# Performance work log

Hardware: AMD Instinct MI355X
Metric: run time of the kernel (lower is better)

The kernel has to match this reference:

```python
import jax, jax.numpy as jnp
import numpy as np

NUM_CLASSES = 21
THRESH = 0.5
VAR = (0.1, 0.2)
B, P, O = 128, 8732, 16

def setup_inputs() -> dict:
    key = jax.random.key(0)
    ks = jax.random.split(key, 7)
    loc_preds = jax.random.normal(ks[0], (B, P, 4), jnp.float32)
    score_preds = jax.random.normal(ks[1], (B, P, NUM_CLASSES), jnp.float32)
    # priors in center-size form (cx, cy, w, h)
    pc = jax.random.uniform(ks[2], (P, 2), minval=0.05, maxval=0.95)
    pwh = jax.random.uniform(ks[3], (P, 2), minval=0.05, maxval=0.4)
    priors = jnp.concatenate([pc, pwh], axis=1).astype(jnp.float32)
    # ground truth: valid point-form boxes + label in last column
    gc = jax.random.uniform(ks[4], (B, O, 2), minval=0.2, maxval=0.8)
    gwh = jax.random.uniform(ks[5], (B, O, 2), minval=0.05, maxval=0.3)
    boxes = jnp.concatenate([gc - gwh / 2, gc + gwh / 2], axis=-1)
    labels = jax.random.randint(ks[6], (B, O, 1), 1, NUM_CLASSES).astype(jnp.float32)
    gt_data = jnp.concatenate([boxes, labels], axis=-1).astype(jnp.float32)
    return {"loc_preds": loc_preds, "score_preds": score_preds,
            "gt_data": gt_data, "priors": priors}

def _iou(a, b):
    # a: (O,4) point form, b: (P,4) point form -> (O,P)
    lt = jnp.maximum(a[:, None, :2], b[None, :, :2])
    rb = jnp.minimum(a[:, None, 2:], b[None, :, 2:])
    wh = jnp.clip(rb - lt, 0.0)
    inter = wh[..., 0] * wh[..., 1]
    area_a = (a[:, 2] - a[:, 0]) * (a[:, 3] - a[:, 1])
    area_b = (b[:, 2] - b[:, 0]) * (b[:, 3] - b[:, 1])
    return inter / (area_a[:, None] + area_b[None, :] - inter)

def _encode(matched, priors):
    # matched: (P,4) point form; priors: (P,4) center-size form
    g_c = (matched[:, :2] + matched[:, 2:]) / 2 - priors[:, :2]
    g_c = g_c / (VAR[0] * priors[:, 2:])
    g_wh = (matched[:, 2:] - matched[:, :2]) / priors[:, 2:]
    g_wh = jnp.log(g_wh) / VAR[1]
    return jnp.concatenate([g_c, g_wh], axis=1)

def _match_one(gt_loc, gt_cls, priors_pt, priors):
    ious = _iou(gt_loc, priors_pt)                    # (O, P)
    best_prior_idx = jnp.argmax(ious, axis=1)         # (O,)
    best_truth_overlap = jnp.max(ious, axis=0)        # (P,)
    best_truth_idx = jnp.argmax(ious, axis=0)         # (P,)
    # ensure every gt's best prior is kept positive and assigned to that gt
    best_truth_overlap = best_truth_overlap.at[best_prior_idx].set(2.0)
    best_truth_idx = best_truth_idx.at[best_prior_idx].set(jnp.arange(gt_loc.shape[0]))
    matched = gt_loc[best_truth_idx]                  # (P, 4)
    conf = gt_cls[best_truth_idx]
    conf = jnp.where(best_truth_overlap < THRESH, 0.0, conf)
    return _encode(matched, priors), conf.astype(jnp.int32)

def reference(loc_preds, score_preds, gt_data, priors):
    priors_pt = jnp.concatenate([priors[:, :2] - priors[:, 2:] / 2,
                                 priors[:, :2] + priors[:, 2:] / 2], axis=1)
    gt_loc, gt_cls = gt_data[..., :4], gt_data[..., 4]
    loc_targets, score_targets = jax.vmap(
        lambda l, c: _match_one(l, c, priors_pt, priors))(gt_loc, gt_cls)
    pos = score_targets > 0                           # (B, P)
    num_matched = jnp.sum(pos).astype(jnp.float32)

    # SmoothL1 over positive boxes (sum reduction)
    d = jnp.abs(loc_preds - loc_targets)
    sl1 = jnp.where(d < 1.0, 0.5 * d * d, d - 0.5)    # (B, P, 4)
    loc_loss = jnp.sum(jnp.where(pos[..., None], sl1, 0.0))

    # per-box cross-entropy on all boxes
    lse = jax.nn.logsumexp(score_preds, axis=-1)      # (B, P)
    gathered = jnp.take_along_axis(score_preds, score_targets[..., None],
                                   axis=-1)[..., 0]
    ce = lse - gathered                               # (B, P)

    # hard negative mining via double argsort ranking
    mine = jnp.where(pos, 0.0, ce)
    idx = jnp.argsort(-mine, axis=1)
    rank = jnp.argsort(idx, axis=1)
    num_pos = jnp.sum(pos, axis=1)                    # (B,)
    total_pos = jnp.sum(num_pos)
    num_neg = jnp.minimum(3 * num_pos, P - total_pos - 1)
    neg = rank < num_neg[:, None]

    sel = pos | neg
    conf_loss = jnp.sum(jnp.where(sel, ce, 0.0))
    return loc_loss / num_matched, conf_loss / num_matched
```

## Files before the change

### kernel.cpp

```cpp
#include <hip/hip_runtime.h>
#include <cstdint>
#include <cstddef>

#define B 128
#define P 8732
#define NC 21
#define O 16
#define THRESH 0.5f
#define QPI 2183
#define NBX 9
#define NPART (B * NBX)
#define NB1 8

typedef unsigned long long u64;
typedef unsigned int u32;
typedef unsigned char u8;

__device__ __forceinline__ float iou_pt(float a0, float a1, float a2, float a3,
                                        float b0, float b1, float b2, float b3) {
    float ltx = fmaxf(a0, b0), lty = fmaxf(a1, b1);
    float rbx = fminf(a2, b2), rby = fminf(a3, b3);
    float wx = fmaxf(rbx - ltx, 0.0f), wy = fmaxf(rby - lty, 0.0f);
    float inter = wx * wy;
    float aa = (a2 - a0) * (a3 - a1);
    float ab = (b2 - b0) * (b3 - b1);
    return inter / (aa + ab - inter);
}

__global__ void __launch_bounds__(256) k_pass1(const float* __restrict__ gt,
                                               const float* __restrict__ priors,
                                               u64* __restrict__ bk,
                                               u8* __restrict__ bidx) {
    const int b = blockIdx.y;
    __shared__ float s_gt[O * 4];
    __shared__ u64 s_wk[4][O];
    const int tid = threadIdx.x;
    const int wave = tid >> 6, lane = tid & 63;
    if (tid < O * 4) {
        int o = tid >> 2, c = tid & 3;
        s_gt[tid] = gt[(b * O + o) * 5 + c];
    }
    __syncthreads();

    u64 lk[O];
#pragma unroll
    for (int o = 0; o < O; o++) lk[o] = 0ull;

    for (int p = blockIdx.x * 256 + tid; p < P; p += NB1 * 256) {
        float4 pr = reinterpret_cast<const float4*>(priors)[p];
        float b0 = pr.x - pr.z * 0.5f, b1 = pr.y - pr.w * 0.5f;
        float b2 = pr.x + pr.z * 0.5f, b3 = pr.y + pr.w * 0.5f;
        float bov = -1.0f; int bo = 0;
#pragma unroll
        for (int o = 0; o < O; o++) {
            float v = iou_pt(s_gt[o * 4 + 0], s_gt[o * 4 + 1], s_gt[o * 4 + 2], s_gt[o * 4 + 3],
                             b0, b1, b2, b3);
            u64 key = ((u64)__float_as_uint(v) << 32) | (u64)(0xFFFFFFFFu - (u32)p);
            lk[o] = (key > lk[o]) ? key : lk[o];
            if (v > bov) { bov = v; bo = o; }
        }
        bidx[(size_t)b * P + p] = (u8)(bo | ((bov >= THRESH) ? 0x80 : 0));
    }

#pragma unroll
    for (int o = 0; o < O; o++) {
        u64 k = lk[o];
#pragma unroll
        for (int off = 32; off > 0; off >>= 1) {
            u64 other = (u64)__shfl_xor((long long)k, off, 64);
            k = (other > k) ? other : k;
        }
        if (lane == 0) s_wk[wave][o] = k;
    }
    __syncthreads();
    if (tid < O) {
        u64 k = s_wk[0][tid];
#pragma unroll
        for (int w = 1; w < 4; w++) { u64 v = s_wk[w][tid]; k = (v > k) ? v : k; }
        bk[((size_t)b * O + tid) * NB1 + blockIdx.x] = k;
    }
}

__global__ void __launch_bounds__(256) k_pass2(const float* __restrict__ gt,
                                               const float* __restrict__ priors,
                                               const u64* __restrict__ bk,
                                               const u8* __restrict__ bidx,
                                               const float* __restrict__ loc_preds,
                                               const float* __restrict__ scores,
                                               float* __restrict__ mine,
                                               double* __restrict__ pl,
                                               double* __restrict__ pc,
                                               int* __restrict__ pn) {
    const int b = blockIdx.y;
    __shared__ float s_gt[O * 5];
    __shared__ int s_bp[O];
    const int tid = threadIdx.x;
    if (tid < O * 5) s_gt[tid] = gt[b * O * 5 + tid];
    if (tid < O) {
        u64 k = bk[((size_t)b * O + tid) * NB1];
#pragma unroll
        for (int i = 1; i < NB1; i++) {
            u64 v = bk[((size_t)b * O + tid) * NB1 + i];
            k = (v > k) ? v : k;
        }
        s_bp[tid] = (int)(0xFFFFFFFFu - (u32)(k & 0xFFFFFFFFull));
    }
    __syncthreads();

    const int gq = blockIdx.x * 256 + tid;
    double l_loc = 0.0, l_ce = 0.0;
    int l_np = 0;

    if (gq < QPI) {
        const int p0 = gq * 4;
        float fs[84];
        const float4* s4 = reinterpret_cast<const float4*>(scores)
                           + (size_t)b * (size_t)(P * NC / 4) + (size_t)21 * gq;
#pragma unroll
        for (int i = 0; i < 21; i++) {
            float4 v = s4[i];
            fs[4 * i + 0] = v.x; fs[4 * i + 1] = v.y;
            fs[4 * i + 2] = v.z; fs[4 * i + 3] = v.w;
        }
        const u32 mw = *reinterpret_cast<const u32*>(bidx + (size_t)b * P + p0);
        float4 pr4[4];
#pragma unroll
        for (int j = 0; j < 4; j++) pr4[j] = reinterpret_cast<const float4*>(priors)[p0 + j];

        float mine_v[4];

#pragma unroll
        for (int j = 0; j < 4; j++) {
            const int p = p0 + j;
            const float4 pr = pr4[j];

            int e = (int)((mw >> (8 * j)) & 0xFFu);
            int best_idx = e & 0x3F;
            bool matched = (e & 0x80) != 0;
#pragma unroll
            for (int o = 0; o < O; o++) {
                if (s_bp[o] == p) { best_idx = o; matched = true; }
            }
            int cls = matched ? (int)s_gt[best_idx * 5 + 4] : 0;

            float mx = fs[21 * j];
#pragma unroll
            for (int c = 1; c < NC; c++) mx = fmaxf(mx, fs[21 * j + c]);
            float se = 0.0f;
#pragma unroll
            for (int c = 0; c < NC; c++) se += __expf(fs[21 * j + c] - mx);
            float lse = mx + __logf(se);
            float g = fs[21 * j];
#pragma unroll
            for (int c = 1; c < NC; c++) g = (c == cls) ? fs[21 * j + c] : g;
            float ce = lse - g;

            bool pos = cls > 0;
            mine_v[j] = pos ? 0.0f : ce;

            if (pos) {
                l_np++;
                l_ce += (double)ce;
                float m0 = s_gt[best_idx * 5 + 0], m1 = s_gt[best_idx * 5 + 1];
                float m2 = s_gt[best_idx * 5 + 2], m3 = s_gt[best_idx * 5 + 3];
                float tx = ((m0 + m2) * 0.5f - pr.x) / (0.1f * pr.z);
                float ty = ((m1 + m3) * 0.5f - pr.y) / (0.1f * pr.w);
                float tw = __logf((m2 - m0) / pr.z) * 5.0f;
                float th = __logf((m3 - m1) / pr.w) * 5.0f;
                float4 lp = reinterpret_cast<const float4*>(loc_preds)[(size_t)b * P + p];
                float d0 = fabsf(lp.x - tx), d1 = fabsf(lp.y - ty);
                float d2 = fabsf(lp.z - tw), d3 = fabsf(lp.w - th);
                float s0 = d0 < 1.0f ? 0.5f * d0 * d0 : d0 - 0.5f;
                float s1 = d1 < 1.0f ? 0.5f * d1 * d1 : d1 - 0.5f;
                float s2 = d2 < 1.0f ? 0.5f * d2 * d2 : d2 - 0.5f;
                float s3 = d3 < 1.0f ? 0.5f * d3 * d3 : d3 - 0.5f;
                l_loc += (double)(s0 + s1 + s2 + s3);
            }
        }
        float4 mv = make_float4(mine_v[0], mine_v[1], mine_v[2], mine_v[3]);
        reinterpret_cast<float4*>(mine)[((size_t)b * P + p0) >> 2] = mv;
    }

    const int lane = tid & 63;
    const int wave = tid >> 6;
#pragma unroll
    for (int off = 32; off > 0; off >>= 1) {
        l_loc += __shfl_xor(l_loc, off, 64);
        l_ce  += __shfl_xor(l_ce, off, 64);
        l_np  += __shfl_xor(l_np, off, 64);
    }
    __shared__ double s_loc[4], s_ce[4];
    __shared__ int s_np[4];
    if (lane == 0) { s_loc[wave] = l_loc; s_ce[wave] = l_ce; s_np[wave] = l_np; }
    __syncthreads();
    if (tid == 0) {
        int q = b * NBX + blockIdx.x;
        pl[q] = (s_loc[0] + s_loc[1]) + (s_loc[2] + s_loc[3]);
        pc[q] = (s_ce[0] + s_ce[1]) + (s_ce[2] + s_ce[3]);
        pn[q] = s_np[0] + s_np[1] + s_np[2] + s_np[3];
    }
}

__global__ void __launch_bounds__(1024) k_hardneg(const float* __restrict__ mine,
                                                  const int* __restrict__ pn,
                                                  double* __restrict__ pneg) {
    const int b = blockIdx.x;
    const int tid = threadIdx.x;
    const int lane = tid & 63, wave = tid >> 6;
    __shared__ float s_mine[P];
    __shared__ u32 s_hist[256];
    __shared__ u32 s_sel[2];
    __shared__ double s_red[16];
    __shared__ int s_ti[16];
    __shared__ int s_np9[NBX];
    __shared__ int s_k;

    {
        int t = 0;
        for (int i = tid; i < NPART; i += 1024) t += pn[i];
#pragma unroll
        for (int off = 32; off > 0; off >>= 1) t += __shfl_xor(t, off, 64);
        if (lane == 0) s_ti[wave] = t;
    }
    if (tid < NBX) s_np9[tid] = pn[b * NBX + tid];
    __syncthreads();
    if (tid == 0) {
        int tp = 0;
#pragma unroll
        for (int w = 0; w < 16; w++) tp += s_ti[w];
        int np = 0;
#pragma unroll
        for (int x = 0; x < NBX; x++) np += s_np9[x];
        int k = 3 * np;
        int cap = P - tp - 1;
        if (cap < k) k = cap;
        s_k = k;
    }
    __syncthreads();
    const int k = s_k;

    if (k <= 0) {
        if (tid == 0) pneg[b] = 0.0;
        return;
    }

    for (int i = tid; i < P; i += 1024) s_mine[i] = mine[(size_t)b * P + i];
    if (tid == 0) { s_sel[0] = 0u; s_sel[1] = (u32)k; }
    __syncthreads();

    for (int shift = 24; shift >= 0; shift -= 8) {
        if (tid < 256) s_hist[tid] = 0u;
        __syncthreads();
        u32 prefix = s_sel[0];
        u32 kr = s_sel[1];
        u32 himask = (shift == 24) ? 0u : (0xFFFFFFFFu << (shift + 8));
        for (int i = tid; i < P; i += 1024) {
            u32 v = __float_as_uint(s_mine[i]);
            if ((v & himask) == prefix) atomicAdd(&s_hist[(v >> shift) & 255u], 1u);
        }
        __syncthreads();
        if (tid < 64) {
            const int L = tid;
            const int btop = 255 - 4 * L;
            u32 h0 = s_hist[btop], h1 = s_hist[btop - 1], h2 = s_hist[btop - 2], h3 = s_hist[btop - 3];
            u32 g4 = h0 + h1 + h2 + h3;
            u32 x = g4;
#pragma unroll
            for (int off = 1; off < 64; off <<= 1) {
                u32 v = __shfl_up(x, off, 64);
                if (L >= off) x += v;
            }
            u32 excl = x - g4;
            if (excl < kr && excl + g4 >= kr) {
                u32 c = excl; int chosen = btop; u32 kloc = kr;
                u32 nc;
                nc = c + h0; if (c < kr && nc >= kr) { chosen = btop;     kloc = kr - c; } c = nc;
                nc = c + h1; if (c < kr && nc >= kr) { chosen = btop - 1; kloc = kr - c; } c = nc;
                nc = c + h2; if (c < kr && nc >= kr) { chosen = btop - 2; kloc = kr - c; } c = nc;
                nc = c + h3; if (c < kr && nc >= kr) { chosen = btop - 3; kloc = kr - c; } c = nc;
                s_sel[0] = prefix | ((u32)chosen << shift);
                s_sel[1] = kloc;
            }
        }
        __syncthreads();
    }

    u32 tbits = s_sel[0];
    u32 kr = s_sel[1];
    float T = __uint_as_float(tbits);

    double sd = 0.0;
    for (int i = tid; i < P; i += 1024) {
        u32 v = __float_as_uint(s_mine[i]);
        if (v > tbits) sd += (double)s_mine[i];
    }
#pragma unroll
    for (int off = 32; off > 0; off >>= 1) sd += __shfl_xor(sd, off, 64);
    if (lane == 0) s_red[wave] = sd;
    __syncthreads();
    if (tid == 0) {
        double tt = 0.0;
#pragma unroll
        for (int w = 0; w < 16; w++) tt += s_red[w];
        pneg[b] = tt + (double)kr * (double)T;
    }
}

__global__ void __launch_bounds__(1024) k_fin(const double* __restrict__ pl,
                                              const double* __restrict__ pc,
                                              const int* __restrict__ pn,
                                              const double* __restrict__ pneg,
                                              float* __restrict__ out) {
    const int tid = threadIdx.x;
    const int lane = tid & 63, wave = tid >> 6;
    __shared__ double s_l[16], s_c[16], s_g[16];
    __shared__ int s_t[16];

    double tl = 0.0, tc = 0.0, tg = 0.0;
    int tn = 0;
    for (int i = tid; i < NPART; i += 1024) { tl += pl[i]; tc += pc[i]; tn += pn[i]; }
    if (tid < B) tg = pneg[tid];
#pragma unroll
    for (int off = 32; off > 0; off >>= 1) {
        tl += __shfl_xor(tl, off, 64);
        tc += __shfl_xor(tc, off, 64);
        tg += __shfl_xor(tg, off, 64);
        tn += __shfl_xor(tn, off, 64);
    }
    if (lane == 0) { s_l[wave] = tl; s_c[wave] = tc; s_g[wave] = tg; s_t[wave] = tn; }
    __syncthreads();
    if (tid == 0) {
        double al = 0.0, ac = 0.0, ag = 0.0;
        int an = 0;
#pragma unroll
        for (int w = 0; w < 16; w++) { al += s_l[w]; ac += s_c[w]; ag += s_g[w]; an += s_t[w]; }
        double n = (double)an;
        out[0] = (float)(al / n);
        out[1] = (float)((ac + ag) / n);
    }
}

extern "C" void kernel_launch(void* const* d_in, const int* in_sizes, int n_in,
                              void* d_out, int out_size, void* d_ws, size_t ws_size,
                              hipStream_t stream) {
    const float* loc_preds = (const float*)d_in[0];
    const float* scores    = (const float*)d_in[1];
    const float* gt        = (const float*)d_in[2];
    const float* priors    = (const float*)d_in[3];

    char* ws = (char*)d_ws;
    u64* bk      = (u64*)ws;
    double* pl   = (double*)(ws + 131072);
    double* pc   = (double*)(ws + 140288);
    int* pn      = (int*)(ws + 149504);
    double* pneg = (double*)(ws + 154112);
    u8* bidx     = (u8*)(ws + 155136);
    float* mine  = (float*)(ws + 1272832);


    k_pass1<<<dim3(NB1, B), dim3(256), 0, stream>>>(gt, priors, bk, bidx);
    k_pass2<<<dim3(NBX, B), dim3(256), 0, stream>>>(
        gt, priors, bk, bidx, loc_preds, scores, mine, pl, pc, pn);
    k_hardneg<<<dim3(B), dim3(1024), 0, stream>>>(mine, pn, pneg);
    k_fin<<<dim3(1), dim3(1024), 0, stream>>>(pl, pc, pn, pneg, (float*)d_out);
}
```

Baseline: 59.41 us.

## Stage score slabs into LDS with double-buffered async global_load_lds in pass2

Reworks k_pass2 so each wave owns a contiguous run of priors and streams the score rows for 64 priors at a time into per-wave LDS double buffers via global_load_lds. The next chunk's load is issued while the current one is computed. Each lane now handles one prior instead of four, which cuts register pressure from the 84-float array. The aim is better coalescing and overlap of the dominant score read. The cost is extra LDS traffic, manual waitcnt handling, and fewer blocks (6 per batch instead of 9).

Result: no change. 58.27 us (-1.9%).

```diff
diff --git a/kernel.cpp b/kernel.cpp
--- a/kernel.cpp
+++ b/kernel.cpp
@@ -7,10 +7,12 @@
 #define NC 21
 #define O 16
 #define THRESH 0.5f
-#define QPI 2183
-#define NBX 9
-#define NPART (B * NBX)
 #define NB1 8
+#define NBX2 6
+#define BPB 1456
+#define WPW 364
+#define NPART (B * NBX2)
+#define SLABF 1536
 
 typedef unsigned long long u64;
 typedef unsigned int u32;
@@ -81,6 +83,21 @@
     }
 }
 
+__device__ __forceinline__ void stage64(const float* __restrict__ gsrc,
+                                        float* lds, int nf4, int lane) {
+    const char* src = (const char*)gsrc;
+    char* dst = (char*)lds;
+#pragma unroll
+    for (int i = 0; i < 6; i++) {
+        int idx = i * 64 + lane;
+        if (idx >= nf4) idx = nf4 - 1;
+        __builtin_amdgcn_global_load_lds(
+            (const __attribute__((address_space(1))) u32*)(src + (size_t)idx * 16),
+            (__attribute__((address_space(3))) u32*)(dst + i * 1024),
+            16, 0, 0);
+    }
+}
+
 __global__ void __launch_bounds__(256) k_pass2(const float* __restrict__ gt,
                                                const float* __restrict__ priors,
                                                const u64* __restrict__ bk,
@@ -92,9 +109,12 @@
                                                double* __restrict__ pc,
                                                int* __restrict__ pn) {
     const int b = blockIdx.y;
+    const int tid = threadIdx.x;
+    const int wave = tid >> 6, lane = tid & 63;
+    __shared__ float s_slab[4][2][SLABF];
     __shared__ float s_gt[O * 5];
     __shared__ int s_bp[O];
-    const int tid = threadIdx.x;
+
     if (tid < O * 5) s_gt[tid] = gt[b * O * 5 + tid];
     if (tid < O) {
         u64 k = bk[((size_t)b * O + tid) * NB1];
@@ -107,82 +127,88 @@
     }
     __syncthreads();
 
-    const int gq = blockIdx.x * 256 + tid;
+    const int wbase = blockIdx.x * BPB + wave * WPW;
+    int wp = P - wbase; if (wp > WPW) wp = WPW;
+    const int nchunk = (wp > 0) ? ((wp + 63) >> 6) : 0;
+
     double l_loc = 0.0, l_ce = 0.0;
     int l_np = 0;
 
-    if (gq < QPI) {
-        const int p0 = gq * 4;
-        float fs[84];
-        const float4* s4 = reinterpret_cast<const float4*>(scores)
-                           + (size_t)b * (size_t)(P * NC / 4) + (size_t)21 * gq;
-#pragma unroll
-        for (int i = 0; i < 21; i++) {
-            float4 v = s4[i];
-            fs[4 * i + 0] = v.x; fs[4 * i + 1] = v.y;
-            fs[4 * i + 2] = v.z; fs[4 * i + 3] = v.w;
-        }
-        const u32 mw = *reinterpret_cast<const u32*>(bidx + (size_t)b * P + p0);
-        float4 pr4[4];
-#pragma unroll
-        for (int j = 0; j < 4; j++) pr4[j] = reinterpret_cast<const float4*>(priors)[p0 + j];
-
-        float mine_v[4];
-
-#pragma unroll
-        for (int j = 0; j < 4; j++) {
-            const int p = p0 + j;
-            const float4 pr = pr4[j];
-
-            int e = (int)((mw >> (8 * j)) & 0xFFu);
-            int best_idx = e & 0x3F;
-            bool matched = (e & 0x80) != 0;
-#pragma unroll
-            for (int o = 0; o < O; o++) {
-                if (s_bp[o] == p) { best_idx = o; matched = true; }
+    if (nchunk > 0) {
+        {
+            int nv0 = wp < 64 ? wp : 64;
+            stage64(scores + ((size_t)b * P + wbase) * NC,
+                    &s_slab[wave][0][0], nv0 * 21 / 4, lane);
+        }
+        for (int c = 0; c < nchunk; ++c) {
+            const int base = wbase + c * 64;
+            int nv = wp - c * 64; if (nv > 64) nv = 64;
+
+            if (c + 1 < nchunk) {
+                int nv2 = wp - (c + 1) * 64; if (nv2 > 64) nv2 = 64;
+                asm volatile("s_waitcnt lgkmcnt(0)" ::: "memory");
+                stage64(scores + ((size_t)b * P + base + 64) * NC,
+                        &s_slab[wave][(c + 1) & 1][0], nv2 * 21 / 4, lane);
+                asm volatile("s_waitcnt vmcnt(6)" ::: "memory");
+            } else {
+                asm volatile("s_waitcnt vmcnt(0)" ::: "memory");
             }
-            int cls = matched ? (int)s_gt[best_idx * 5 + 4] : 0;
-
-            float mx = fs[21 * j];
-#pragma unroll
-            for (int c = 1; c < NC; c++) mx = fmaxf(mx, fs[21 * j + c]);
-            float se = 0.0f;
-#pragma unroll
-            for (int c = 0; c < NC; c++) se += __expf(fs[21 * j + c] - mx);
-            float lse = mx + __logf(se);
-            float g = fs[21 * j];
-#pragma unroll
-            for (int c = 1; c < NC; c++) g = (c == cls) ? fs[21 * j + c] : g;
-            float ce = lse - g;
-
-            bool pos = cls > 0;
-            mine_v[j] = pos ? 0.0f : ce;
-
-            if (pos) {
-                l_np++;
-                l_ce += (double)ce;
-                float m0 = s_gt[best_idx * 5 + 0], m1 = s_gt[best_idx * 5 + 1];
-                float m2 = s_gt[best_idx * 5 + 2], m3 = s_gt[best_idx * 5 + 3];
-                float tx = ((m0 + m2) * 0.5f - pr.x) / (0.1f * pr.z);
-                float ty = ((m1 + m3) * 0.5f - pr.y) / (0.1f * pr.w);
-                float tw = __logf((m2 - m0) / pr.z) * 5.0f;
-                float th = __logf((m3 - m1) / pr.w) * 5.0f;
-                float4 lp = reinterpret_cast<const float4*>(loc_preds)[(size_t)b * P + p];
-                float d0 = fabsf(lp.x - tx), d1 = fabsf(lp.y - ty);
-                float d2 = fabsf(lp.z - tw), d3 = fabsf(lp.w - th);
-                float s0 = d0 < 1.0f ? 0.5f * d0 * d0 : d0 - 0.5f;
-                float s1 = d1 < 1.0f ? 0.5f * d1 * d1 : d1 - 0.5f;
-                float s2 = d2 < 1.0f ? 0.5f * d2 * d2 : d2 - 0.5f;
-                float s3 = d3 < 1.0f ? 0.5f * d3 * d3 : d3 - 0.5f;
-                l_loc += (double)(s0 + s1 + s2 + s3);
+            __builtin_amdgcn_sched_barrier(0);
+
+            if (lane < nv) {
+                const int p = base + lane;
+                const float* fsl = &s_slab[wave][c & 1][lane * NC];
+                float fs[NC];
+#pragma unroll
+                for (int cc = 0; cc < NC; cc++) fs[cc] = fsl[cc];
+
+                int e = (int)bidx[(size_t)b * P + p];
+                int best_idx = e & 0x3F;
+                bool matched = (e & 0x80) != 0;
+#pragma unroll
+                for (int o = 0; o < O; o++) {
+                    if (s_bp[o] == p) { best_idx = o; matched = true; }
+                }
+                int cls = matched ? (int)s_gt[best_idx * 5 + 4] : 0;
+
+                float mx = fs[0];
+#pragma unroll
+                for (int cc = 1; cc < NC; cc++) mx = fmaxf(mx, fs[cc]);
+                float se = 0.0f;
+#pragma unroll
+                for (int cc = 0; cc < NC; cc++) se += __expf(fs[cc] - mx);
+                float lse = mx + __logf(se);
+                float g = fs[0];
+#pragma unroll
+                for (int cc = 1; cc < NC; cc++) g = (cc == cls) ? fs[cc] : g;
+                float ce = lse - g;
+
+                bool pos = cls > 0;
+                mine[(size_t)b * P + p] = pos ? 0.0f : ce;
+
+                if (pos) {
+                    l_np++;
+                    l_ce += (double)ce;
+                    float4 pr = reinterpret_cast<const float4*>(priors)[p];
+                    float m0 = s_gt[best_idx * 5 + 0], m1 = s_gt[best_idx * 5 + 1];
+                    float m2 = s_gt[best_idx * 5 + 2], m3 = s_gt[best_idx * 5 + 3];
+                    float tx = ((m0 + m2) * 0.5f - pr.x) / (0.1f * pr.z);
+                    float ty = ((m1 + m3) * 0.5f - pr.y) / (0.1f * pr.w);
+                    float tw = __logf((m2 - m0) / pr.z) * 5.0f;
+                    float th = __logf((m3 - m1) / pr.w) * 5.0f;
+                    float4 lp = reinterpret_cast<const float4*>(loc_preds)[(size_t)b * P + p];
+                    float d0 = fabsf(lp.x - tx), d1 = fabsf(lp.y - ty);
+                    float d2 = fabsf(lp.z - tw), d3 = fabsf(lp.w - th);
+                    float s0 = d0 < 1.0f ? 0.5f * d0 * d0 : d0 - 0.5f;
+                    float s1 = d1 < 1.0f ? 0.5f * d1 * d1 : d1 - 0.5f;
+                    float s2 = d2 < 1.0f ? 0.5f * d2 * d2 : d2 - 0.5f;
+                    float s3 = d3 < 1.0f ? 0.5f * d3 * d3 : d3 - 0.5f;
+                    l_loc += (double)((s0 + s1) + (s2 + s3));
+                }
             }
         }
-        float4 mv = make_float4(mine_v[0], mine_v[1], mine_v[2], mine_v[3]);
-        reinterpret_cast<float4*>(mine)[((size_t)b * P + p0) >> 2] = mv;
-    }
-
-    const int lane = tid & 63;
-    const int wave = tid >> 6;
+    }
+
 #pragma unroll
     for (int off = 32; off > 0; off >>= 1) {
         l_loc += __shfl_xor(l_loc, off, 64);
@@ -194,7 +220,7 @@
     if (lane == 0) { s_loc[wave] = l_loc; s_ce[wave] = l_ce; s_np[wave] = l_np; }
     __syncthreads();
     if (tid == 0) {
-        int q = b * NBX + blockIdx.x;
+        int q = b * NBX2 + blockIdx.x;
         pl[q] = (s_loc[0] + s_loc[1]) + (s_loc[2] + s_loc[3]);
         pc[q] = (s_ce[0] + s_ce[1]) + (s_ce[2] + s_ce[3]);
         pn[q] = s_np[0] + s_np[1] + s_np[2] + s_np[3];
@@ -212,7 +238,7 @@
     __shared__ u32 s_sel[2];
     __shared__ double s_red[16];
     __shared__ int s_ti[16];
-    __shared__ int s_np9[NBX];
+    __shared__ int s_npx[NBX2];
     __shared__ int s_k;
 
     {
@@ -222,7 +248,7 @@
         for (int off = 32; off > 0; off >>= 1) t += __shfl_xor(t, off, 64);
         if (lane == 0) s_ti[wave] = t;
     }
-    if (tid < NBX) s_np9[tid] = pn[b * NBX + tid];
+    if (tid < NBX2) s_npx[tid] = pn[b * NBX2 + tid];
     __syncthreads();
     if (tid == 0) {
         int tp = 0;
@@ -230,7 +256,7 @@
         for (int w = 0; w < 16; w++) tp += s_ti[w];
         int np = 0;
 #pragma unroll
-        for (int x = 0; x < NBX; x++) np += s_np9[x];
+        for (int x = 0; x < NBX2; x++) np += s_npx[x];
         int k = 3 * np;
         int cap = P - tp - 1;
         if (cap < k) k = cap;
@@ -351,15 +377,15 @@
     char* ws = (char*)d_ws;
     u64* bk      = (u64*)ws;
     double* pl   = (double*)(ws + 131072);
-    double* pc   = (double*)(ws + 140288);
-    int* pn      = (int*)(ws + 149504);
-    double* pneg = (double*)(ws + 154112);
-    u8* bidx     = (u8*)(ws + 155136);
-    float* mine  = (float*)(ws + 1272832);
+    double* pc   = (double*)(ws + 137216);
+    int* pn      = (int*)(ws + 143360);
+    double* pneg = (double*)(ws + 146432);
+    u8* bidx     = (u8*)(ws + 147456);
+    float* mine  = (float*)(ws + 1265152);
 
 
     k_pass1<<<dim3(NB1, B), dim3(256), 0, stream>>>(gt, priors, bk, bidx);
-    k_pass2<<<dim3(NBX, B), dim3(256), 0, stream>>>(
+    k_pass2<<<dim3(NBX2, B), dim3(256), 0, stream>>>(
         gt, priors, bk, bidx, loc_preds, scores, mine, pl, pc, pn);
     k_hardneg<<<dim3(B), dim3(1024), 0, stream>>>(mine, pn, pneg);
     k_fin<<<dim3(1), dim3(1024), 0, stream>>>(pl, pc, pn, pneg, (float*)d_out);
```

## Move forced-match merge into tiny kernel and lighten pass2 per-prior work

Applied to the files above, without the earlier changes.

Adds a single-block k_merge kernel that reduces the per-block best-prior keys and writes the forced matches directly into the per-prior bidx byte map. k_pass2 no longer reloads bk or runs the 16-way per-prior compare loop. It loads priors only for positive boxes, skips the class gather for unmatched priors, and accumulates partial sums in float instead of double. The cost is an extra kernel launch and a serial dependency. Float accumulation may slightly change rounding, and a forced match whose gt label is zero would now count as positive.

Measured after the change: 66.08 us. 11.2% more time.

```diff
diff --git a/kernel.cpp b/kernel.cpp
--- a/kernel.cpp
+++ b/kernel.cpp
@@ -81,9 +81,29 @@
     }
 }
 
+__global__ void __launch_bounds__(128) k_merge(const u64* __restrict__ bk,
+                                               u8* __restrict__ bidx) {
+    const int b = threadIdx.x;
+    u64 kk[O];
+#pragma unroll
+    for (int o = 0; o < O; o++) {
+        u64 k = bk[((size_t)b * O + o) * NB1];
+#pragma unroll
+        for (int i = 1; i < NB1; i++) {
+            u64 v = bk[((size_t)b * O + o) * NB1 + i];
+            k = (v > k) ? v : k;
+        }
+        kk[o] = k;
+    }
+#pragma unroll
+    for (int o = 0; o < O; o++) {
+        int p = (int)(0xFFFFFFFFu - (u32)(kk[o] & 0xFFFFFFFFull));
+        bidx[(size_t)b * P + p] = (u8)(o | 0x80);
+    }
+}
+
 __global__ void __launch_bounds__(256) k_pass2(const float* __restrict__ gt,
                                                const float* __restrict__ priors,
-                                               const u64* __restrict__ bk,
                                                const u8* __restrict__ bidx,
                                                const float* __restrict__ loc_preds,
                                                const float* __restrict__ scores,
@@ -93,22 +113,12 @@
                                                int* __restrict__ pn) {
     const int b = blockIdx.y;
     __shared__ float s_gt[O * 5];
-    __shared__ int s_bp[O];
     const int tid = threadIdx.x;
     if (tid < O * 5) s_gt[tid] = gt[b * O * 5 + tid];
-    if (tid < O) {
-        u64 k = bk[((size_t)b * O + tid) * NB1];
-#pragma unroll
-        for (int i = 1; i < NB1; i++) {
-            u64 v = bk[((size_t)b * O + tid) * NB1 + i];
-            k = (v > k) ? v : k;
-        }
-        s_bp[tid] = (int)(0xFFFFFFFFu - (u32)(k & 0xFFFFFFFFull));
-    }
     __syncthreads();
 
     const int gq = blockIdx.x * 256 + tid;
-    double l_loc = 0.0, l_ce = 0.0;
+    float l_loc = 0.f, l_ce = 0.f;
     int l_np = 0;
 
     if (gq < QPI) {
@@ -123,24 +133,16 @@
             fs[4 * i + 2] = v.z; fs[4 * i + 3] = v.w;
         }
         const u32 mw = *reinterpret_cast<const u32*>(bidx + (size_t)b * P + p0);
-        float4 pr4[4];
-#pragma unroll
-        for (int j = 0; j < 4; j++) pr4[j] = reinterpret_cast<const float4*>(priors)[p0 + j];
 
         float mine_v[4];
 
 #pragma unroll
         for (int j = 0; j < 4; j++) {
             const int p = p0 + j;
-            const float4 pr = pr4[j];
 
             int e = (int)((mw >> (8 * j)) & 0xFFu);
             int best_idx = e & 0x3F;
             bool matched = (e & 0x80) != 0;
-#pragma unroll
-            for (int o = 0; o < O; o++) {
-                if (s_bp[o] == p) { best_idx = o; matched = true; }
-            }
             int cls = matched ? (int)s_gt[best_idx * 5 + 4] : 0;
 
             float mx = fs[21 * j];
@@ -150,17 +152,18 @@
 #pragma unroll
             for (int c = 0; c < NC; c++) se += __expf(fs[21 * j + c] - mx);
             float lse = mx + __logf(se);
-            float g = fs[21 * j];
-#pragma unroll
-            for (int c = 1; c < NC; c++) g = (c == cls) ? fs[21 * j + c] : g;
-            float ce = lse - g;
-
-            bool pos = cls > 0;
-            mine_v[j] = pos ? 0.0f : ce;
-
-            if (pos) {
+
+            if (!matched) {
+                mine_v[j] = lse - fs[21 * j];
+            } else {
+                mine_v[j] = 0.0f;
+                float g = fs[21 * j + 1];
+#pragma unroll
+                for (int c = 2; c < NC; c++) g = (c == cls) ? fs[21 * j + c] : g;
+                float ce = lse - g;
                 l_np++;
-                l_ce += (double)ce;
+                l_ce += ce;
+                float4 pr = reinterpret_cast<const float4*>(priors)[p];
                 float m0 = s_gt[best_idx * 5 + 0], m1 = s_gt[best_idx * 5 + 1];
                 float m2 = s_gt[best_idx * 5 + 2], m3 = s_gt[best_idx * 5 + 3];
                 float tx = ((m0 + m2) * 0.5f - pr.x) / (0.1f * pr.z);
@@ -174,7 +177,7 @@
                 float s1 = d1 < 1.0f ? 0.5f * d1 * d1 : d1 - 0.5f;
                 float s2 = d2 < 1.0f ? 0.5f * d2 * d2 : d2 - 0.5f;
                 float s3 = d3 < 1.0f ? 0.5f * d3 * d3 : d3 - 0.5f;
-                l_loc += (double)(s0 + s1 + s2 + s3);
+                l_loc += (s0 + s1) + (s2 + s3);
             }
         }
         float4 mv = make_float4(mine_v[0], mine_v[1], mine_v[2], mine_v[3]);
@@ -191,7 +194,7 @@
     }
     __shared__ double s_loc[4], s_ce[4];
     __shared__ int s_np[4];
-    if (lane == 0) { s_loc[wave] = l_loc; s_ce[wave] = l_ce; s_np[wave] = l_np; }
+    if (lane == 0) { s_loc[wave] = (double)l_loc; s_ce[wave] = (double)l_ce; s_np[wave] = l_np; }
     __syncthreads();
     if (tid == 0) {
         int q = b * NBX + blockIdx.x;
@@ -212,7 +215,7 @@
     __shared__ u32 s_sel[2];
     __shared__ double s_red[16];
     __shared__ int s_ti[16];
-    __shared__ int s_np9[NBX];
+    __shared__ int s_npx[NBX];
     __shared__ int s_k;
 
     {
@@ -222,7 +225,7 @@
         for (int off = 32; off > 0; off >>= 1) t += __shfl_xor(t, off, 64);
         if (lane == 0) s_ti[wave] = t;
     }
-    if (tid < NBX) s_np9[tid] = pn[b * NBX + tid];
+    if (tid < NBX) s_npx[tid] = pn[b * NBX + tid];
     __syncthreads();
     if (tid == 0) {
         int tp = 0;
@@ -230,7 +233,7 @@
         for (int w = 0; w < 16; w++) tp += s_ti[w];
         int np = 0;
 #pragma unroll
-        for (int x = 0; x < NBX; x++) np += s_np9[x];
+        for (int x = 0; x < NBX; x++) np += s_npx[x];
         int k = 3 * np;
         int cap = P - tp - 1;
         if (cap < k) k = cap;
@@ -359,8 +362,9 @@
 
 
     k_pass1<<<dim3(NB1, B), dim3(256), 0, stream>>>(gt, priors, bk, bidx);
+    k_merge<<<dim3(1), dim3(128), 0, stream>>>(bk, bidx);
     k_pass2<<<dim3(NBX, B), dim3(256), 0, stream>>>(
-        gt, priors, bk, bidx, loc_preds, scores, mine, pl, pc, pn);
+        gt, priors, bidx, loc_preds, scores, mine, pl, pc, pn);
     k_hardneg<<<dim3(B), dim3(1024), 0, stream>>>(mine, pn, pneg);
     k_fin<<<dim3(1), dim3(1024), 0, stream>>>(pl, pc, pn, pneg, (float*)d_out);
 }
```

## Split pass2 quads across two threads and fuse final reduction into hardneg

Applied to the files above, without the earlier changes.

Each 4-prior quad in pass2 is now handled by two threads, each processing two priors. Each thread loads 11 float4 of scores instead of 21, and the grid doubles to 18 blocks in x, which is meant to raise parallelism and lower register pressure. Per-thread accumulation switches from double to float. The separate k_fin launch is removed: hardneg blocks atomically add their negative sums to a global double and take a ticket, and the last block does the final reduction. This drops one kernel launch at the cost of atomics and slightly different float rounding.

Result: slower. 87.58 us (+47.4%).

```diff
diff --git a/kernel.cpp b/kernel.cpp
--- a/kernel.cpp
+++ b/kernel.cpp
@@ -8,7 +8,7 @@
 #define O 16
 #define THRESH 0.5f
 #define QPI 2183
-#define NBX 9
+#define NBX 18
 #define NPART (B * NBX)
 #define NB1 8
 
@@ -30,12 +30,15 @@
 __global__ void __launch_bounds__(256) k_pass1(const float* __restrict__ gt,
                                                const float* __restrict__ priors,
                                                u64* __restrict__ bk,
-                                               u8* __restrict__ bidx) {
+                                               u8* __restrict__ bidx,
+                                               double* __restrict__ acc,
+                                               u32* __restrict__ ticket) {
     const int b = blockIdx.y;
     __shared__ float s_gt[O * 4];
     __shared__ u64 s_wk[4][O];
     const int tid = threadIdx.x;
     const int wave = tid >> 6, lane = tid & 63;
+    if (blockIdx.x == 0 && b == 0 && tid == 0) { acc[0] = 0.0; *ticket = 0u; }
     if (tid < O * 4) {
         int o = tid >> 2, c = tid & 3;
         s_gt[tid] = gt[(b * O + o) * 5 + c];
@@ -79,6 +82,57 @@
         for (int w = 1; w < 4; w++) { u64 v = s_wk[w][tid]; k = (v > k) ? v : k; }
         bk[((size_t)b * O + tid) * NB1 + blockIdx.x] = k;
     }
+}
+
+template<int OFF>
+__device__ __forceinline__ float prior_eval(const float (&fq)[44],
+                                            const float* s_gt, const int* s_bp,
+                                            int p, int ebyte,
+                                            const float* __restrict__ priors,
+                                            const float* __restrict__ loc_preds,
+                                            size_t lp_base,
+                                            float& l_loc, float& l_ce, int& l_np) {
+    int best_idx = ebyte & 0x3F;
+    bool matched = (ebyte & 0x80) != 0;
+#pragma unroll
+    for (int o = 0; o < O; o++) {
+        if (s_bp[o] == p) { best_idx = o; matched = true; }
+    }
+    int cls = matched ? (int)s_gt[best_idx * 5 + 4] : 0;
+
+    float mx = fq[OFF];
+#pragma unroll
+    for (int c = 1; c < NC; c++) mx = fmaxf(mx, fq[OFF + c]);
+    float se = 0.0f;
+#pragma unroll
+    for (int c = 0; c < NC; c++) se += __expf(fq[OFF + c] - mx);
+    float lse = mx + __logf(se);
+    float g = fq[OFF];
+#pragma unroll
+    for (int c = 1; c < NC; c++) g = (c == cls) ? fq[OFF + c] : g;
+    float ce = lse - g;
+
+    if (matched) {
+        l_np++;
+        l_ce += ce;
+        float4 pr = reinterpret_cast<const float4*>(priors)[p];
+        float m0 = s_gt[best_idx * 5 + 0], m1 = s_gt[best_idx * 5 + 1];
+        float m2 = s_gt[best_idx * 5 + 2], m3 = s_gt[best_idx * 5 + 3];
+        float tx = ((m0 + m2) * 0.5f - pr.x) / (0.1f * pr.z);
+        float ty = ((m1 + m3) * 0.5f - pr.y) / (0.1f * pr.w);
+        float tw = __logf((m2 - m0) / pr.z) * 5.0f;
+        float th = __logf((m3 - m1) / pr.w) * 5.0f;
+        float4 lp = reinterpret_cast<const float4*>(loc_preds)[lp_base + p];
+        float d0 = fabsf(lp.x - tx), d1 = fabsf(lp.y - ty);
+        float d2 = fabsf(lp.z - tw), d3 = fabsf(lp.w - th);
+        float s0 = d0 < 1.0f ? 0.5f * d0 * d0 : d0 - 0.5f;
+        float s1 = d1 < 1.0f ? 0.5f * d1 * d1 : d1 - 0.5f;
+        float s2 = d2 < 1.0f ? 0.5f * d2 * d2 : d2 - 0.5f;
+        float s3 = d3 < 1.0f ? 0.5f * d3 * d3 : d3 - 0.5f;
+        l_loc += (s0 + s1) + (s2 + s3);
+        return 0.0f;
+    }
+    return ce;
 }
 
 __global__ void __launch_bounds__(256) k_pass2(const float* __restrict__ gt,
@@ -107,78 +161,38 @@
     }
     __syncthreads();
 
-    const int gq = blockIdx.x * 256 + tid;
-    double l_loc = 0.0, l_ce = 0.0;
+    const int h = tid >> 7;
+    const int qi = blockIdx.x * 128 + (tid & 127);
+    float l_loc = 0.f, l_ce = 0.f;
     int l_np = 0;
 
-    if (gq < QPI) {
-        const int p0 = gq * 4;
-        float fs[84];
+    if (qi < QPI) {
         const float4* s4 = reinterpret_cast<const float4*>(scores)
-                           + (size_t)b * (size_t)(P * NC / 4) + (size_t)21 * gq;
-#pragma unroll
-        for (int i = 0; i < 21; i++) {
+                           + (size_t)b * (size_t)(P * NC / 4) + (size_t)21 * qi + h * 10;
+        float fq[44];
+#pragma unroll
+        for (int i = 0; i < 11; i++) {
             float4 v = s4[i];
-            fs[4 * i + 0] = v.x; fs[4 * i + 1] = v.y;
-            fs[4 * i + 2] = v.z; fs[4 * i + 3] = v.w;
-        }
-        const u32 mw = *reinterpret_cast<const u32*>(bidx + (size_t)b * P + p0);
-        float4 pr4[4];
-#pragma unroll
-        for (int j = 0; j < 4; j++) pr4[j] = reinterpret_cast<const float4*>(priors)[p0 + j];
-
-        float mine_v[4];
-
-#pragma unroll
-        for (int j = 0; j < 4; j++) {
-            const int p = p0 + j;
-            const float4 pr = pr4[j];
-
-            int e = (int)((mw >> (8 * j)) & 0xFFu);
-            int best_idx = e & 0x3F;
-            bool matched = (e & 0x80) != 0;
-#pragma unroll
-            for (int o = 0; o < O; o++) {
-                if (s_bp[o] == p) { best_idx = o; matched = true; }
-            }
-            int cls = matched ? (int)s_gt[best_idx * 5 + 4] : 0;
-
-            float mx = fs[21 * j];
-#pragma unroll
-            for (int c = 1; c < NC; c++) mx = fmaxf(mx, fs[21 * j + c]);
-            float se = 0.0f;
-#pragma unroll
-            for (int c = 0; c < NC; c++) se += __expf(fs[21 * j + c] - mx);
-            float lse = mx + __logf(se);
-            float g = fs[21 * j];
-#pragma unroll
-            for (int c = 1; c < NC; c++) g = (c == cls) ? fs[21 * j + c] : g;
-            float ce = lse - g;
-
-            bool pos = cls > 0;
-            mine_v[j] = pos ? 0.0f : ce;
-
-            if (pos) {
-                l_np++;
-                l_ce += (double)ce;
-                float m0 = s_gt[best_idx * 5 + 0], m1 = s_gt[best_idx * 5 + 1];
-                float m2 = s_gt[best_idx * 5 + 2], m3 = s_gt[best_idx * 5 + 3];
-                float tx = ((m0 + m2) * 0.5f - pr.x) / (0.1f * pr.z);
-                float ty = ((m1 + m3) * 0.5f - pr.y) / (0.1f * pr.w);
-                float tw = __logf((m2 - m0) / pr.z) * 5.0f;
-                float th = __logf((m3 - m1) / pr.w) * 5.0f;
-                float4 lp = reinterpret_cast<const float4*>(loc_preds)[(size_t)b * P + p];
-                float d0 = fabsf(lp.x - tx), d1 = fabsf(lp.y - ty);
-                float d2 = fabsf(lp.z - tw), d3 = fabsf(lp.w - th);
-                float s0 = d0 < 1.0f ? 0.5f * d0 * d0 : d0 - 0.5f;
-                float s1 = d1 < 1.0f ? 0.5f * d1 * d1 : d1 - 0.5f;
-                float s2 = d2 < 1.0f ? 0.5f * d2 * d2 : d2 - 0.5f;
-                float s3 = d3 < 1.0f ? 0.5f * d3 * d3 : d3 - 0.5f;
-                l_loc += (double)(s0 + s1 + s2 + s3);
-            }
-        }
-        float4 mv = make_float4(mine_v[0], mine_v[1], mine_v[2], mine_v[3]);
-        reinterpret_cast<float4*>(mine)[((size_t)b * P + p0) >> 2] = mv;
+            fq[4 * i + 0] = v.x; fq[4 * i + 1] = v.y;
+            fq[4 * i + 2] = v.z; fq[4 * i + 3] = v.w;
+        }
+        const int p0 = 4 * qi + 2 * h;
+        const u32 mw = *reinterpret_cast<const unsigned short*>(bidx + (size_t)b * P + p0);
+        const size_t lp_base = (size_t)b * P;
+
+        float2 mv;
+        if (h == 0) {
+            mv.x = prior_eval<0>(fq, s_gt, s_bp, p0, (int)(mw & 0xFFu),
+                                 priors, loc_preds, lp_base, l_loc, l_ce, l_np);
+            mv.y = prior_eval<21>(fq, s_gt, s_bp, p0 + 1, (int)(mw >> 8),
+                                  priors, loc_preds, lp_base, l_loc, l_ce, l_np);
+        } else {
+            mv.x = prior_eval<2>(fq, s_gt, s_bp, p0, (int)(mw & 0xFFu),
+                                 priors, loc_preds, lp_base, l_loc, l_ce, l_np);
+            mv.y = prior_eval<23>(fq, s_gt, s_bp, p0 + 1, (int)(mw >> 8),
+                                  priors, loc_preds, lp_base, l_loc, l_ce, l_np);
+        }
+        *reinterpret_cast<float2*>(mine + (size_t)b * P + p0) = mv;
     }
 
     const int lane = tid & 63;
@@ -191,7 +205,7 @@
     }
     __shared__ double s_loc[4], s_ce[4];
     __shared__ int s_np[4];
-    if (lane == 0) { s_loc[wave] = l_loc; s_ce[wave] = l_ce; s_np[wave] = l_np; }
+    if (lane == 0) { s_loc[wave] = (double)l_loc; s_ce[wave] = (double)l_ce; s_np[wave] = l_np; }
     __syncthreads();
     if (tid == 0) {
         int q = b * NBX + blockIdx.x;
@@ -202,8 +216,12 @@
 }
 
 __global__ void __launch_bounds__(1024) k_hardneg(const float* __restrict__ mine,
+                                                  const double* __restrict__ pl,
+                                                  const double* __restrict__ pc,
                                                   const int* __restrict__ pn,
-                                                  double* __restrict__ pneg) {
+                                                  double* __restrict__ acc,
+                                                  u32* __restrict__ ticket,
+                                                  float* __restrict__ out) {
     const int b = blockIdx.x;
     const int tid = threadIdx.x;
     const int lane = tid & 63, wave = tid >> 6;
@@ -212,8 +230,7 @@
     __shared__ u32 s_sel[2];
     __shared__ double s_red[16];
     __shared__ int s_ti[16];
-    __shared__ int s_np9[NBX];
-    __shared__ int s_k;
+    __shared__ int s_k, s_tp;
 
     {
         int t = 0;
@@ -222,121 +239,111 @@
         for (int off = 32; off > 0; off >>= 1) t += __shfl_xor(t, off, 64);
         if (lane == 0) s_ti[wave] = t;
     }
-    if (tid < NBX) s_np9[tid] = pn[b * NBX + tid];
     __syncthreads();
     if (tid == 0) {
         int tp = 0;
 #pragma unroll
         for (int w = 0; w < 16; w++) tp += s_ti[w];
         int np = 0;
-#pragma unroll
-        for (int x = 0; x < NBX; x++) np += s_np9[x];
+        for (int x = 0; x < NBX; x++) np += pn[b * NBX + x];
         int k = 3 * np;
         int cap = P - tp - 1;
         if (cap < k) k = cap;
         s_k = k;
+        s_tp = tp;
     }
     __syncthreads();
     const int k = s_k;
 
-    if (k <= 0) {
-        if (tid == 0) pneg[b] = 0.0;
-        return;
-    }
-
-    for (int i = tid; i < P; i += 1024) s_mine[i] = mine[(size_t)b * P + i];
-    if (tid == 0) { s_sel[0] = 0u; s_sel[1] = (u32)k; }
-    __syncthreads();
-
-    for (int shift = 24; shift >= 0; shift -= 8) {
-        if (tid < 256) s_hist[tid] = 0u;
+    if (k > 0) {
+        for (int i = tid; i < P; i += 1024) s_mine[i] = mine[(size_t)b * P + i];
+        if (tid == 0) { s_sel[0] = 0u; s_sel[1] = (u32)k; }
         __syncthreads();
-        u32 prefix = s_sel[0];
+
+        for (int shift = 24; shift >= 0; shift -= 8) {
+            if (tid < 256) s_hist[tid] = 0u;
+            __syncthreads();
+            u32 prefix = s_sel[0];
+            u32 kr = s_sel[1];
+            u32 himask = (shift == 24) ? 0u : (0xFFFFFFFFu << (shift + 8));
+            for (int i = tid; i < P; i += 1024) {
+                u32 v = __float_as_uint(s_mine[i]);
+                if ((v & himask) == prefix) atomicAdd(&s_hist[(v >> shift) & 255u], 1u);
+            }
+            __syncthreads();
+            if (tid < 64) {
+                const int L = tid;
+                const int btop = 255 - 4 * L;
+                u32 h0 = s_hist[btop], h1 = s_hist[btop - 1], h2 = s_hist[btop - 2], h3 = s_hist[btop - 3];
+                u32 g4 = h0 + h1 + h2 + h3;
+                u32 x = g4;
+#pragma unroll
+                for (int off = 1; off < 64; off <<= 1) {
+                    u32 v = __shfl_up(x, off, 64);
+                    if (L >= off) x += v;
+                }
+                u32 excl = x - g4;
+                if (excl < kr && excl + g4 >= kr) {
+                    u32 c = excl; int chosen = btop; u32 kloc = kr;
+                    u32 nc;
+                    nc = c + h0; if (c < kr && nc >= kr) { chosen = btop;     kloc = kr - c; } c = nc;
+                    nc = c + h1; if (c < kr && nc >= kr) { chosen = btop - 1; kloc = kr - c; } c = nc;
+                    nc = c + h2; if (c < kr && nc >= kr) { chosen = btop - 2; kloc = kr - c; } c = nc;
+                    nc = c + h3; if (c < kr && nc >= kr) { chosen = btop - 3; kloc = kr - c; } c = nc;
+                    s_sel[0] = prefix | ((u32)chosen << shift);
+                    s_sel[1] = kloc;
+                }
+            }
+            __syncthreads();
+        }
+
+        u32 tbits = s_sel[0];
         u32 kr = s_sel[1];
-        u32 himask = (shift == 24) ? 0u : (0xFFFFFFFFu << (shift + 8));
+        float T = __uint_as_float(tbits);
+
+        double sd = 0.0;
         for (int i = tid; i < P; i += 1024) {
             u32 v = __float_as_uint(s_mine[i]);
-            if ((v & himask) == prefix) atomicAdd(&s_hist[(v >> shift) & 255u], 1u);
-        }
+            if (v > tbits) sd += (double)s_mine[i];
+        }
+#pragma unroll
+        for (int off = 32; off > 0; off >>= 1) sd += __shfl_xor(sd, off, 64);
+        if (lane == 0) s_red[wave] = sd;
         __syncthreads();
-        if (tid < 64) {
-            const int L = tid;
-            const int btop = 255 - 4 * L;
-            u32 h0 = s_hist[btop], h1 = s_hist[btop - 1], h2 = s_hist[btop - 2], h3 = s_hist[btop - 3];
-            u32 g4 = h0 + h1 + h2 + h3;
-            u32 x = g4;
-#pragma unroll
-            for (int off = 1; off < 64; off <<= 1) {
-                u32 v = __shfl_up(x, off, 64);
-                if (L >= off) x += v;
-            }
-            u32 excl = x - g4;
-            if (excl < kr && excl + g4 >= kr) {
-                u32 c = excl; int chosen = btop; u32 kloc = kr;
-                u32 nc;
-                nc = c + h0; if (c < kr && nc >= kr) { chosen = btop;     kloc = kr - c; } c = nc;
-                nc = c + h1; if (c < kr && nc >= kr) { chosen = btop - 1; kloc = kr - c; } c = nc;
-                nc = c + h2; if (c < kr && nc >= kr) { chosen = btop - 2; kloc = kr - c; } c = nc;
-                nc = c + h3; if (c < kr && nc >= kr) { chosen = btop - 3; kloc = kr - c; } c = nc;
-                s_sel[0] = prefix | ((u32)chosen << shift);
-                s_sel[1] = kloc;
-            }
-        }
+        if (tid == 0) {
+            double tt = 0.0;
+#pragma unroll
+            for (int w = 0; w < 16; w++) tt += s_red[w];
+            atomicAdd(&acc[0], tt + (double)kr * (double)T);
+        }
+    }
+
+    __threadfence();
+    __syncthreads();
+    __shared__ int s_last;
+    if (tid == 0) s_last = (atomicAdd(ticket, 1u) == B - 1) ? 1 : 0;
+    __syncthreads();
+    if (s_last) {
+        __shared__ double f_l[16], f_c[16];
+        double tl = 0.0, tc = 0.0;
+        for (int i = tid; i < NPART; i += 1024) { tl += pl[i]; tc += pc[i]; }
+#pragma unroll
+        for (int off = 32; off > 0; off >>= 1) {
+            tl += __shfl_xor(tl, off, 64);
+            tc += __shfl_xor(tc, off, 64);
+        }
+        if (lane == 0) { f_l[wave] = tl; f_c[wave] = tc; }
         __syncthreads();
-    }
-
-    u32 tbits = s_sel[0];
-    u32 kr = s_sel[1];
-    float T = __uint_as_float(tbits);
-
-    double sd = 0.0;
-    for (int i = tid; i < P; i += 1024) {
-        u32 v = __float_as_uint(s_mine[i]);
-        if (v > tbits) sd += (double)s_mine[i];
-    }
-#pragma unroll
-    for (int off = 32; off > 0; off >>= 1) sd += __shfl_xor(sd, off, 64);
-    if (lane == 0) s_red[wave] = sd;
-    __syncthreads();
-    if (tid == 0) {
-        double tt = 0.0;
-#pragma unroll
-        for (int w = 0; w < 16; w++) tt += s_red[w];
-        pneg[b] = tt + (double)kr * (double)T;
-    }
-}
-
-__global__ void __launch_bounds__(1024) k_fin(const double* __restrict__ pl,
-                                              const double* __restrict__ pc,
-                                              const int* __restrict__ pn,
-                                              const double* __restrict__ pneg,
-                                              float* __restrict__ out) {
-    const int tid = threadIdx.x;
-    const int lane = tid & 63, wave = tid >> 6;
-    __shared__ double s_l[16], s_c[16], s_g[16];
-    __shared__ int s_t[16];
-
-    double tl = 0.0, tc = 0.0, tg = 0.0;
-    int tn = 0;
-    for (int i = tid; i < NPART; i += 1024) { tl += pl[i]; tc += pc[i]; tn += pn[i]; }
-    if (tid < B) tg = pneg[tid];
-#pragma unroll
-    for (int off = 32; off > 0; off >>= 1) {
-        tl += __shfl_xor(tl, off, 64);
-        tc += __shfl_xor(tc, off, 64);
-        tg += __shfl_xor(tg, off, 64);
-        tn += __shfl_xor(tn, off, 64);
-    }
-    if (lane == 0) { s_l[wave] = tl; s_c[wave] = tc; s_g[wave] = tg; s_t[wave] = tn; }
-    __syncthreads();
-    if (tid == 0) {
-        double al = 0.0, ac = 0.0, ag = 0.0;
-        int an = 0;
-#pragma unroll
-        for (int w = 0; w < 16; w++) { al += s_l[w]; ac += s_c[w]; ag += s_g[w]; an += s_t[w]; }
-        double n = (double)an;
-        out[0] = (float)(al / n);
-        out[1] = (float)((ac + ag) / n);
+        if (tid == 0) {
+            double al = 0.0, ac = 0.0;
+#pragma unroll
+            for (int w = 0; w < 16; w++) { al += f_l[w]; ac += f_c[w]; }
+            __threadfence();
+            double ag = atomicAdd(&acc[0], 0.0);
+            double n = (double)s_tp;
+            out[0] = (float)(al / n);
+            out[1] = (float)((ac + ag) / n);
+        }
     }
 }
 
@@ -351,16 +358,16 @@
     char* ws = (char*)d_ws;
     u64* bk      = (u64*)ws;
     double* pl   = (double*)(ws + 131072);
-    double* pc   = (double*)(ws + 140288);
-    int* pn      = (int*)(ws + 149504);
-    double* pneg = (double*)(ws + 154112);
-    u8* bidx     = (u8*)(ws + 155136);
-    float* mine  = (float*)(ws + 1272832);
-
-
-    k_pass1<<<dim3(NB1, B), dim3(256), 0, stream>>>(gt, priors, bk, bidx);
+    double* pc   = (double*)(ws + 149504);
+    int* pn      = (int*)(ws + 167936);
+    double* acc  = (double*)(ws + 177152);
+    u32* ticket  = (u32*)(ws + 177160);
+    u8* bidx     = (u8*)(ws + 177168);
+    float* mine  = (float*)(ws + 1294880);
+
+    k_pass1<<<dim3(NB1, B), dim3(256), 0, stream>>>(gt, priors, bk, bidx, acc, ticket);
     k_pass2<<<dim3(NBX, B), dim3(256), 0, stream>>>(
         gt, priors, bk, bidx, loc_preds, scores, mine, pl, pc, pn);
-    k_hardneg<<<dim3(B), dim3(1024), 0, stream>>>(mine, pn, pneg);
-    k_fin<<<dim3(1), dim3(1024), 0, stream>>>(pl, pc, pn, pneg, (float*)d_out);
-}
+    k_hardneg<<<dim3(B), dim3(1024), 0, stream>>>(mine, pl, pc, pn, acc, ticket,
+                                                  (float*)d_out);
+}
```
